# Kernel tuning notes

Hardware: AMD Instinct MI355X
Metric: run time of the kernel (lower is better)

Reference implementation:

```python
import jax, jax.numpy as jnp
import numpy as np
from jax import lax

L = 2048        # leaves per tree
VOCAB = 50000
IN_DIM = 300
MEM = 150
HID = 50
NCLS = 5


def _balanced_tree(n_leaf):
    # children-before-parent topological order; node ids: [0, n_leaf) leaves,
    # [n_leaf, 2*n_leaf-1) internal, last id is the root's single child (ROOT is passthrough).
    level = list(range(n_leaf)); nid = n_leaf; lefts = []; rights = []
    while len(level) > 1:
        nxt = []
        for j in range(0, len(level) - 1, 2):
            lefts.append(level[j]); rights.append(level[j + 1]); nxt.append(nid); nid += 1
        if len(level) % 2:
            nxt.append(level[-1])
        level = nxt
    return np.asarray(lefts, np.int32), np.asarray(rights, np.int32)


def setup_inputs() -> dict:
    key = jax.random.key(0)
    ks = jax.random.split(key, 12)
    left, right = _balanced_tree(L)
    s = 0.05
    return {
        "l_tokens": jax.random.randint(ks[0], (L,), 0, VOCAB, dtype=jnp.int32),
        "r_tokens": jax.random.randint(ks[1], (L,), 0, VOCAB, dtype=jnp.int32),
        "left_idx": jnp.asarray(left),
        "right_idx": jnp.asarray(right),
        "emb": jax.random.normal(ks[2], (VOCAB, IN_DIM), jnp.float32) * s,
        "W_ioux": jax.random.normal(ks[3], (IN_DIM, 3 * MEM), jnp.float32) * s,
        "b_ioux": jnp.zeros((3 * MEM,), jnp.float32),
        "W_iouh": jax.random.normal(ks[4], (MEM, 3 * MEM), jnp.float32) * s,
        "b_iouh": jnp.zeros((3 * MEM,), jnp.float32),
        "W_fx": jax.random.normal(ks[5], (IN_DIM, MEM), jnp.float32) * s,
        "b_fx": jnp.zeros((MEM,), jnp.float32),
        "W_fh": jax.random.normal(ks[6], (MEM, MEM), jnp.float32) * s,
        "b_fh": jnp.zeros((MEM,), jnp.float32),
        "W_attn": jax.random.normal(ks[7], (2 * MEM, MEM), jnp.float32) * s,
        "b_attn": jnp.zeros((MEM,), jnp.float32),
        "W_wh": jax.random.normal(ks[8], (2 * MEM, HID), jnp.float32) * s,
        "b_wh": jnp.zeros((HID,), jnp.float32),
        "W_wp": jax.random.normal(ks[9], (HID, NCLS), jnp.float32) * s,
        "b_wp": jnp.zeros((NCLS,), jnp.float32),
    }


def _gates(iou):
    i, o, u = jnp.split(iou, 3, axis=-1)
    return jax.nn.sigmoid(i), jax.nn.sigmoid(o), jnp.tanh(u)


def _tree_lstm(tokens, left, right, emb, W_ioux, b_ioux, W_iouh, b_iouh, W_fh, b_fh):
    # Leaves (child_c = child_h = 0): iou = ioux(x) + iouh(0); fc term vanishes.
    x = emb[tokens]                                   # [L, in_dim]
    i, o, u = _gates(x @ W_ioux + b_ioux + b_iouh)
    c_leaf = i * u
    h_leaf = o * jnp.tanh(c_leaf)
    n_leaf = tokens.shape[0]
    N = 2 * n_leaf - 1
    C = jnp.zeros((N, MEM), x.dtype).at[:n_leaf].set(c_leaf)
    H = jnp.zeros((N, MEM), x.dtype).at[:n_leaf].set(h_leaf)

    # Internal nodes (inputs=None branch): iou = iouh(sum h_child); f_k = sigmoid(fh(h_k)).
    def step(carry, inp):
        C, H = carry
        k, li, ri = inp
        hl, hr = H[li], H[ri]
        i, o, u = _gates((hl + hr) @ W_iouh + b_iouh)
        fl = jax.nn.sigmoid(hl @ W_fh + b_fh)
        fr = jax.nn.sigmoid(hr @ W_fh + b_fh)
        c = i * u + fl * C[li] + fr * C[ri]
        h = o * jnp.tanh(c)
        return (C.at[k].set(c), H.at[k].set(h)), None

    ids = jnp.arange(n_leaf, N, dtype=jnp.int32)
    (C, H), _ = lax.scan(step, (C, H), (ids, left, right))
    return H  # [N, MEM]; H[-1] is the root hidden state (ROOT is passthrough)


def reference(l_tokens, r_tokens, left_idx, right_idx, emb, W_ioux, b_ioux, W_iouh, b_iouh, W_fx, b_fx, W_fh, b_fh, W_attn, b_attn, W_wh, b_wh, W_wp, b_wp):
    Hl = _tree_lstm(l_tokens, left_idx, right_idx, emb, W_ioux, b_ioux, W_iouh, b_iouh, W_fh, b_fh)
    Hr = _tree_lstm(r_tokens, left_idx, right_idx, emb, W_ioux, b_ioux, W_iouh, b_iouh, W_fh, b_fh)
    # Soft cross-attention over all node hidden states (torch code builds [Nr,Nl,m] beta;
    # here expressed as matmuls -- identical math).
    scores = Hl @ Hr.T                               # [Nl, Nr]
    beta_sum = jax.nn.softmax(scores, axis=1) @ Hr    # [Nl, MEM]
    alpha_sum = jax.nn.softmax(scores.T, axis=1) @ Hl  # [Nr, MEM]
    v_l = jnp.concatenate([Hl, beta_sum], axis=1) @ W_attn + b_attn
    v_r = jnp.concatenate([Hr, alpha_sum], axis=1) @ W_attn + b_attn
    lh = v_l[-1:]  # root hidden (root_idx is the root's matched row)
    rh = v_r[-1:]
    feats = jnp.concatenate([lh * rh, jnp.abs(lh - rh)], axis=1)
    hid = jax.nn.sigmoid(feats @ W_wh + b_wh)
    return jax.nn.log_softmax(hid @ W_wp + b_wp, axis=-1)  # [1, NCLS]
```

## Files before the change

kernel.cpp:

```cpp
#include <hip/hip_runtime.h>
#include <math.h>

#define LEAVES 2048
#define NN     4095
#define MEMD   150
#define IOUD   450
#define IND    300
#define STR    152
#define CT     4096
#define NT     29
#define KT     10
#define KT5    5
#define NTW    39
#define LTILES 49
#define OUTSTR 788

__device__ __forceinline__ float sigf(float x) { return 1.f / (1.f + expf(-x)); }

__device__ __forceinline__ unsigned short f2bf(float v) {
    union { float f; unsigned u; } x; x.f = v;
    unsigned r = x.u + 0x7fffu + ((x.u >> 16) & 1u);
    return (unsigned short)(r >> 16);
}

typedef short bf16x8 __attribute__((ext_vector_type(8)));
typedef float f32x4  __attribute__((ext_vector_type(4)));

#define J_PW  22500
#define J_PB  (NT * KT * 64)
#define J_PBW (NTW * KT5 * 64)
#define J_XB  (4096 * 80)
__global__ __launch_bounds__(256) void k_prep(
    const float* __restrict__ Wh, const float* __restrict__ Wf,
    const float* __restrict__ Wx,
    const int* __restrict__ ltok, const int* __restrict__ rtok,
    const float* __restrict__ emb,
    float4* __restrict__ PWhf, unsigned short* __restrict__ PB,
    unsigned short* __restrict__ PBW, unsigned short* __restrict__ Xb)
{
    int i = blockIdx.x * 256 + threadIdx.x;
    if (i < J_PW) {
        int k = i / 150, d = i - k * 150;
        float4 v;
        v.x = Wh[k * IOUD + d];
        v.y = Wh[k * IOUD + 150 + d];
        v.z = Wh[k * IOUD + 300 + d];
        v.w = Wf[k * MEMD + d];
        PWhf[i] = v;
    } else if (i < J_PW + J_PB) {
        int j2 = i - J_PW;
        int nt = j2 / (KT * 64);
        int rem = j2 - nt * (KT * 64);
        int kt = rem >> 6, l = rem & 63;
        int jc = nt * 16 + (l & 15);
        int kb = kt * 32 + ((l >> 4) << 3);
        unsigned short o[8];
        #pragma unroll
        for (int e = 0; e < 8; ++e) {
            int k = kb + e;
            float v = (k < IND && jc < IOUD) ? Wx[k * IOUD + jc] : 0.f;
            o[e] = f2bf(v);
        }
        *(ushort4*)(PB + (size_t)j2 * 8)     = make_ushort4(o[0], o[1], o[2], o[3]);
        *(ushort4*)(PB + (size_t)j2 * 8 + 4) = make_ushort4(o[4], o[5], o[6], o[7]);
    } else if (i < J_PW + J_PB + J_PBW) {
        int j3 = i - J_PW - J_PB;
        int bt = j3 / (KT5 * 64);
        int rem = j3 - bt * (KT5 * 64);
        int kt = rem >> 6, l = rem & 63;
        int jc = bt * 16 + (l & 15);
        int kb = kt * 32 + ((l >> 4) << 3);
        unsigned short o[8];
        #pragma unroll
        for (int e = 0; e < 8; ++e) {
            int k = kb + e;
            float v = 0.f;
            if (k < MEMD) {
                if (jc < IOUD)                  v = Wh[k * IOUD + jc];
                else if (jc >= 464 && jc < 614) v = Wf[k * MEMD + (jc - 464)];
            }
            o[e] = f2bf(v);
        }
        *(ushort4*)(PBW + (size_t)j3 * 8)     = make_ushort4(o[0], o[1], o[2], o[3]);
        *(ushort4*)(PBW + (size_t)j3 * 8 + 4) = make_ushort4(o[4], o[5], o[6], o[7]);
    } else if (i < J_PW + J_PB + J_PBW + J_XB) {
        int idx = i - J_PW - J_PB - J_PBW;
        int row = idx / 80, q = idx - row * 80;
        int kb = q * 4;
        int leaf = row & 2047, tree = row >> 11;
        int tk = (tree ? rtok : ltok)[leaf];
        unsigned short o[4];
        #pragma unroll
        for (int e = 0; e < 4; ++e) {
            int k = kb + e;
            float v = (k < IND) ? emb[(size_t)tk * IND + k] : 0.f;
            o[e] = f2bf(v);
        }
        *(ushort4*)(Xb + (size_t)row * 320 + kb) = make_ushort4(o[0], o[1], o[2], o[3]);
    }
}

__global__ __launch_bounds__(512) void k_leafg(
    const unsigned short* __restrict__ Xb, const unsigned short* __restrict__ PB,
    const float* __restrict__ bx, const float* __restrict__ bh,
    float* __restrict__ C, float* __restrict__ H)
{
    __shared__ float ioub[16][464];
    const int t = threadIdx.x, w = t >> 6, l = t & 63;
    const int mt = blockIdx.x;

    const short* Ap = (const short*)Xb + (size_t)(mt * 16 + (l & 15)) * 320 + ((l >> 4) << 3);
    for (int nt = w; nt < NT; nt += 8) {
        const short* Bp = (const short*)PB + (size_t)nt * (KT * 512) + l * 8;
        f32x4 acc = {0.f, 0.f, 0.f, 0.f};
        #pragma unroll
        for (int kt = 0; kt < KT; ++kt) {
            bf16x8 a = *(const bf16x8*)(Ap + kt * 32);
            bf16x8 b = *(const bf16x8*)(Bp + kt * 512);
            acc = __builtin_amdgcn_mfma_f32_16x16x32_bf16(a, b, acc, 0, 0, 0);
        }
        const int col = nt * 16 + (l & 15);
        const int rb  = (l >> 4) << 2;
        #pragma unroll
        for (int r = 0; r < 4; ++r) ioub[rb + r][col] = acc[r];
    }
    __syncthreads();

    for (int idx = t; idx < 16 * MEMD; idx += 512) {
        int m = idx / MEMD, d = idx - m * MEMD;
        int gm = mt * 16 + m;
        int tree = gm >> 11, leaf = gm & 2047;
        float iv = ioub[m][d]       + bx[d]       + bh[d];
        float ov = ioub[m][d + 150] + bx[d + 150] + bh[d + 150];
        float uv = ioub[m][d + 300] + bx[d + 300] + bh[d + 300];
        float c = sigf(iv) * tanhf(uv);
        float h = sigf(ov) * tanhf(c);
        C[((size_t)tree * CT + leaf) * STR + d] = c;
        H[((size_t)tree * CT + leaf) * STR + d] = h;
    }
}

__global__ __launch_bounds__(256) void k_lvlgF(
    const unsigned short* __restrict__ PBW,
    const float* __restrict__ bh, const float* __restrict__ bf,
    float* __restrict__ C, float* __restrict__ H,
    int n, int PB_, int CB)
{
    __shared__ unsigned short AS[KT5 * 64 * 8];
    __shared__ unsigned short AL[KT5 * 64 * 8];
    __shared__ float outb[16][OUTSTR];
    const int t = threadIdx.x;
    const int m0 = blockIdx.x * 16;

    for (int s = t; s < KT5 * 64; s += 256) {
        int kt = s >> 6, l = s & 63;
        int m = m0 + (l & 15);
        int tree = (m >= n) ? 1 : 0;
        int p = m - tree * n;
        const float* rL = H + ((size_t)tree * CT + (CB + 2 * p)) * STR;
        const float* rR = rL + STR;
        int kb = kt * 32 + ((l >> 4) << 3);
        unsigned short hs8[8], hl8[8];
        if (kb + 8 <= MEMD) {
            float4 a0 = *(const float4*)(rL + kb);
            float4 a1 = *(const float4*)(rL + kb + 4);
            float4 b0 = *(const float4*)(rR + kb);
            float4 b1 = *(const float4*)(rR + kb + 4);
            float av[8] = {a0.x,a0.y,a0.z,a0.w,a1.x,a1.y,a1.z,a1.w};
            float bv[8] = {b0.x,b0.y,b0.z,b0.w,b1.x,b1.y,b1.z,b1.w};
            #pragma unroll
            for (int e = 0; e < 8; ++e) {
                hs8[e] = f2bf(av[e] + bv[e]);
                hl8[e] = f2bf(av[e]);
            }
        } else {
            #pragma unroll
            for (int e = 0; e < 8; ++e) {
                int k = kb + e;
                float a = (k < MEMD) ? rL[k] : 0.f;
                float b = (k < MEMD) ? rR[k] : 0.f;
                hs8[e] = f2bf(a + b);
                hl8[e] = f2bf(a);
            }
        }
        *(ushort4*)(AS + (size_t)s * 8)     = make_ushort4(hs8[0], hs8[1], hs8[2], hs8[3]);
        *(ushort4*)(AS + (size_t)s * 8 + 4) = make_ushort4(hs8[4], hs8[5], hs8[6], hs8[7]);
        *(ushort4*)(AL + (size_t)s * 8)     = make_ushort4(hl8[0], hl8[1], hl8[2], hl8[3]);
        *(ushort4*)(AL + (size_t)s * 8 + 4) = make_ushort4(hl8[4], hl8[5], hl8[6], hl8[7]);
    }
    __syncthreads();

    {
        const int w = t >> 6, l = t & 63;
        for (int T = w; T < LTILES; T += 4) {
            const int isHL = (T >= NTW) ? 1 : 0;
            const int bT = isHL ? (T - NTW + 29) : T;
            const unsigned short* As = isHL ? AL : AS;
            const short* Bp = (const short*)PBW + (size_t)bT * (KT5 * 512) + l * 8;
            f32x4 acc = {0.f, 0.f, 0.f, 0.f};
            #pragma unroll
            for (int kt = 0; kt < KT5; ++kt) {
                bf16x8 a = *(const bf16x8*)((const short*)As + (kt * 64 + l) * 8);
                bf16x8 b = *(const bf16x8*)(Bp + kt * 512);
                acc = __builtin_amdgcn_mfma_f32_16x16x32_bf16(a, b, acc, 0, 0, 0);
            }
            const int col = bT * 16 + (l & 15) + (isHL ? 160 : 0);
            const int rb  = (l >> 4) << 2;
            #pragma unroll
            for (int r = 0; r < 4; ++r) outb[rb + r][col] = acc[r];
        }
    }
    __syncthreads();

    for (int idx = t; idx < 16 * MEMD; idx += 256) {
        int m = idx / MEMD, d = idx - m * MEMD;
        int gm = m0 + m;
        int tree = (gm >= n) ? 1 : 0, p = gm - tree * n;
        float* Ct = C + (size_t)tree * CT * STR;
        float* Ht = H + (size_t)tree * CT * STR;
        int c0 = CB + 2 * p;
        float cl = Ct[(size_t)c0 * STR + d];
        float cr = Ct[(size_t)(c0 + 1) * STR + d];
        float iv = outb[m][d]       + bh[d];
        float ov = outb[m][d + 150] + bh[d + 150];
        float uv = outb[m][d + 300] + bh[d + 300];
        float fs = outb[m][464 + d] + 2.f * bf[d];
        float fl = outb[m][624 + d] + bf[d];
        float fr = fs - fl;
        float c = sigf(iv) * tanhf(uv) + sigf(fl) * cl + sigf(fr) * cr;
        float h = sigf(ov) * tanhf(c);
        size_t rw = (size_t)(PB_ + p) * STR + d;
        Ct[rw] = c;
        Ht[rw] = h;
    }
}

__global__ __launch_bounds__(640) void k_node(
    const float4* __restrict__ PWhf, const float* __restrict__ bh,
    const float* __restrict__ bf,
    float* __restrict__ C, float* __restrict__ H, int PB_, int CB)
{
    __shared__ float hsv[MEMD], hlv[MEMD];
    __shared__ float part[4][5][152];
    const int tree = blockIdx.y, node = blockIdx.x, t = threadIdx.x;
    float* Ct = C + (size_t)tree * CT * STR;
    float* Ht = H + (size_t)tree * CT * STR;
    const int c0 = CB + 2 * node;

    if (t < MEMD) {
        float a = Ht[(size_t)c0 * STR + t];
        float b = Ht[(size_t)(c0 + 1) * STR + t];
        hsv[t] = a + b;
        hlv[t] = a;
    }
    __syncthreads();

    const int grp = t / 160, d = t - grp * 160;
    if (d < MEMD) {
        const int k0 = (grp * MEMD) >> 2;
        const int k1 = ((grp + 1) * MEMD) >> 2;
        float ai = 0.f, ao = 0.f, au = 0.f, afs = 0.f, afl = 0.f;
        const float4* wp = PWhf + d;
        #pragma unroll 4
        for (int k = k0; k < k1; ++k) {
            float4 w = wp[(size_t)k * 150];
            float hs = hsv[k], hl = hlv[k];
            ai  = fmaf(hs, w.x, ai);
            ao  = fmaf(hs, w.y, ao);
            au  = fmaf(hs, w.z, au);
            afs = fmaf(hs, w.w, afs);
            afl = fmaf(hl, w.w, afl);
        }
        part[grp][0][d] = ai;  part[grp][1][d] = ao;  part[grp][2][d] = au;
        part[grp][3][d] = afs; part[grp][4][d] = afl;
    }
    __syncthreads();

    if (t < MEMD) {
        const int d2 = t;
        float ai = bh[d2], ao = bh[d2 + 150], au = bh[d2 + 300];
        float bfv = bf[d2];
        float afs = 2.f * bfv, afl = bfv;
        #pragma unroll
        for (int g = 0; g < 4; ++g) {
            ai  += part[g][0][d2]; ao  += part[g][1][d2]; au += part[g][2][d2];
            afs += part[g][3][d2]; afl += part[g][4][d2];
        }
        float cl = Ct[(size_t)c0 * STR + d2];
        float cr = Ct[(size_t)(c0 + 1) * STR + d2];
        float frv = afs - afl;
        float c = sigf(ai) * tanhf(au) + sigf(afl) * cl + sigf(frv) * cr;
        float h = sigf(ao) * tanhf(c);
        size_t rw = (size_t)(PB_ + node) * STR + d2;
        Ct[rw] = c;
        Ht[rw] = h;
    }
}

__global__ __launch_bounds__(256) void k_attn(
    const float* __restrict__ H, float* __restrict__ cstat, float* __restrict__ part)
{
    __shared__ float lv[MEMD];
    __shared__ float sc[64];
    __shared__ float pv[64];
    const int bid = blockIdx.x, t = threadIdx.x;
    const int side = bid >> 6, chunk = bid & 63;
    const int j0 = chunk << 6;
    const int jn = min(64, NN - j0);
    const float* lastrow = H + ((size_t)side * CT + (NN - 1)) * STR;
    if (t < MEMD) lv[t] = lastrow[t];
    __syncthreads();

    const float* src = H + (size_t)(side ^ 1) * CT * STR + (size_t)j0 * STR;
    const int wave = t >> 6, lane = t & 63;
    for (int r = wave; r < jn; r += 4) {
        const float* row = src + (size_t)r * STR;
        float a = lv[lane] * row[lane] + lv[lane + 64] * row[lane + 64];
        if (lane < 22) a += lv[lane + 128] * row[lane + 128];
        #pragma unroll
        for (int off = 32; off; off >>= 1) a += __shfl_xor(a, off);
        if (lane == 0) sc[r] = a;
    }
    __syncthreads();
    if (wave == 0) {
        float v = (lane < jn) ? sc[lane] : -3.4e38f;
        float m = v;
        #pragma unroll
        for (int off = 32; off; off >>= 1) m = fmaxf(m, __shfl_xor(m, off));
        float e = (lane < jn) ? expf(v - m) : 0.f;
        pv[lane] = e;
        float s = e;
        #pragma unroll
        for (int off = 32; off; off >>= 1) s += __shfl_xor(s, off);
        if (lane == 0) {
            cstat[(side * 64 + chunk) * 2 + 0] = m;
            cstat[(side * 64 + chunk) * 2 + 1] = s;
        }
    }
    __syncthreads();
    if (t < MEMD) {
        float a = 0.f;
        for (int j = 0; j < jn; ++j) a += pv[j] * src[(size_t)j * STR + t];
        part[(size_t)(side * 64 + chunk) * STR + t] = a;
    }
}

__global__ __launch_bounds__(512) void k_final(
    const float* __restrict__ H, const float* __restrict__ cstat,
    const float* __restrict__ part,
    const float* __restrict__ Wattn, const float* __restrict__ battn,
    const float* __restrict__ Wwh, const float* __restrict__ bwh,
    const float* __restrict__ Wwp, const float* __restrict__ bwp,
    float* __restrict__ outp)
{
    __shared__ float scl[2][64];
    __shared__ float gseS[2];
    __shared__ float ba[300], catl[300], catr[300], vl[150], vr[150];
    __shared__ float feats[300], hid[50], logits[5];
    const int t = threadIdx.x, wave = t >> 6, lane = t & 63;

    if (wave < 2) {
        float lm = cstat[(wave * 64 + lane) * 2 + 0];
        float ls = cstat[(wave * 64 + lane) * 2 + 1];
        float m = lm;
        #pragma unroll
        for (int off = 32; off; off >>= 1) m = fmaxf(m, __shfl_xor(m, off));
        float s = expf(lm - m);
        scl[wave][lane] = s;
        float se = ls * s;
        #pragma unroll
        for (int off = 32; off; off >>= 1) se += __shfl_xor(se, off);
        if (lane == 0) gseS[wave] = se;
    }
    __syncthreads();
    if (t < 300) {
        int side = t / MEMD, d = t - side * MEMD;
        float a = 0.f;
        for (int c = 0; c < 64; ++c)
            a += part[(size_t)(side * 64 + c) * STR + d] * scl[side][c];
        ba[t] = a / gseS[side];
    }
    __syncthreads();
    const float* Hl_last = H + (size_t)(0 * CT + NN - 1) * STR;
    const float* Hr_last = H + (size_t)(1 * CT + NN - 1) * STR;
    if (t < MEMD) {
        catl[t] = Hl_last[t]; catl[150 + t] = ba[t];
        catr[t] = Hr_last[t]; catr[150 + t] = ba[150 + t];
    }
    __syncthreads();
    if (t < 300) {
        int d = (t < 150) ? t : t - 150;
        const float* cat = (t < 150) ? catl : catr;
        float a = battn[d];
        for (int k = 0; k < 300; ++k) a = fmaf(cat[k], Wattn[k * 150 + d], a);
        if (t < 150) vl[d] = a; else vr[d] = a;
    }
    __syncthreads();
    if (t < MEMD) {
        feats[t] = vl[t] * vr[t];
        feats[150 + t] = fabsf(vl[t] - vr[t]);
    }
    __syncthreads();
    if (t < 50) {
        float a = bwh[t];
        for (int k = 0; k < 300; ++k) a = fmaf(feats[k], Wwh[k * 50 + t], a);
        hid[t] = sigf(a);
    }
    __syncthreads();
    if (t < 5) {
        float a = bwp[t];
        for (int g = 0; g < 50; ++g) a = fmaf(hid[g], Wwp[g * 5 + t], a);
        logits[t] = a;
    }
    __syncthreads();
    if (t == 0) {
        float m = logits[0];
        for (int c = 1; c < 5; ++c) m = fmaxf(m, logits[c]);
        float s = 0.f;
        for (int c = 0; c < 5; ++c) s += expf(logits[c] - m);
        float lse = m + logf(s);
        for (int c = 0; c < 5; ++c) outp[c] = logits[c] - lse;
    }
}

extern "C" void kernel_launch(void* const* d_in, const int* in_sizes, int n_in,
                              void* d_out, int out_size, void* d_ws, size_t ws_size,
                              hipStream_t stream)
{
    const int*   ltok  = (const int*)d_in[0];
    const int*   rtok  = (const int*)d_in[1];
    const float* emb   = (const float*)d_in[4];
    const float* Wx    = (const float*)d_in[5];
    const float* bx    = (const float*)d_in[6];
    const float* Wh    = (const float*)d_in[7];
    const float* bh    = (const float*)d_in[8];
    const float* Wf    = (const float*)d_in[11];
    const float* bf    = (const float*)d_in[12];
    const float* Wattn = (const float*)d_in[13];
    const float* battn = (const float*)d_in[14];
    const float* Wwh   = (const float*)d_in[15];
    const float* bwh   = (const float*)d_in[16];
    const float* Wwp   = (const float*)d_in[17];
    const float* bwp   = (const float*)d_in[18];
    float* out = (float*)d_out;

    float* ws    = (float*)d_ws;
    float*  C    = ws;
    float*  H    = C + (size_t)2 * CT * STR;
    float*  cs   = H + (size_t)2 * CT * STR;
    float*  part = cs + 256;
    float4* PWhf = (float4*)(part + (size_t)128 * STR);
    unsigned short* Xb  = (unsigned short*)(PWhf + 22500);
    unsigned short* PBb = Xb + (size_t)4096 * 320;
    unsigned short* PBW = PBb + (size_t)NT * KT * 512;

    const int prep_items = J_PW + J_PB + J_PBW + J_XB;
    k_prep<<<dim3((prep_items + 255) / 256), dim3(256), 0, stream>>>(
        Wh, Wf, Wx, ltok, rtok, emb, PWhf, PBb, PBW, Xb);

    k_leafg<<<dim3(256), dim3(512), 0, stream>>>(Xb, PBb, bx, bh, C, H);

    k_lvlgF<<<dim3(128), dim3(256), 0, stream>>>(PBW, bh, bf, C, H, 1024, 2048, 0);
    k_lvlgF<<<dim3(64),  dim3(256), 0, stream>>>(PBW, bh, bf, C, H, 512, 3072, 2048);
    k_lvlgF<<<dim3(32),  dim3(256), 0, stream>>>(PBW, bh, bf, C, H, 256, 3584, 3072);

    k_node<<<dim3(128, 2), dim3(640), 0, stream>>>(PWhf, bh, bf, C, H, 3840, 3584);
    k_node<<<dim3(64,  2), dim3(640), 0, stream>>>(PWhf, bh, bf, C, H, 3968, 3840);
    k_node<<<dim3(32,  2), dim3(640), 0, stream>>>(PWhf, bh, bf, C, H, 4032, 3968);
    k_node<<<dim3(16,  2), dim3(640), 0, stream>>>(PWhf, bh, bf, C, H, 4064, 4032);
    k_node<<<dim3(8,   2), dim3(640), 0, stream>>>(PWhf, bh, bf, C, H, 4080, 4064);
    k_node<<<dim3(4,   2), dim3(640), 0, stream>>>(PWhf, bh, bf, C, H, 4088, 4080);
    k_node<<<dim3(2,   2), dim3(640), 0, stream>>>(PWhf, bh, bf, C, H, 4092, 4088);
    k_node<<<dim3(1,   2), dim3(640), 0, stream>>>(PWhf, bh, bf, C, H, 4094, 4092);

    k_attn<<<dim3(128), dim3(256), 0, stream>>>(H, cs, part);
    k_final<<<dim3(1), dim3(512), 0, stream>>>(H, cs, part, Wattn, battn,
                                               Wwh, bwh, Wwp, bwp, out);
}
```

Measured before the change: 142.4 us.

## Fuse last five tree levels into one persistent block per tree

Replaces five small per-level k_node launches for the top of the tree with a single kernel launch in which one 1024-thread block per tree walks the five levels, using __syncthreads between levels. The aim is to remove the launch and inter-kernel gap overhead of tiny kernels. In exchange, each level runs on only one CU per tree, with one thread per (node, dim) doing a full 150-long dot product. That reduces parallelism compared with the split-K k_node design.

```diff
diff --git a/kernel.cpp b/kernel.cpp
--- a/kernel.cpp
+++ b/kernel.cpp
@@ -297,6 +297,62 @@
     }
 }
 
+__global__ __launch_bounds__(1024) void k_tail5(
+    const float4* __restrict__ PWhf, const float* __restrict__ bh,
+    const float* __restrict__ bf,
+    float* __restrict__ C, float* __restrict__ H)
+{
+    __shared__ float hsv[16][152], hlv[16][152];
+    const int tree = blockIdx.x, t = threadIdx.x;
+    float* Ct = C + (size_t)tree * CT * STR;
+    float* Ht = H + (size_t)tree * CT * STR;
+
+    const int ns[5]  = {16, 8, 4, 2, 1};
+    const int cbs[5] = {4032, 4064, 4080, 4088, 4092};
+    const int pbs[5] = {4064, 4080, 4088, 4092, 4094};
+
+    #pragma unroll 1
+    for (int lv = 0; lv < 5; ++lv) {
+        const int n = ns[lv], CB = cbs[lv], PB_ = pbs[lv];
+        for (int idx = t; idx < n * MEMD; idx += 1024) {
+            int p = idx / MEMD, d = idx - p * MEMD;
+            float a = Ht[(size_t)(CB + 2 * p) * STR + d];
+            float b = Ht[(size_t)(CB + 2 * p + 1) * STR + d];
+            hsv[p][d] = a + b;
+            hlv[p][d] = a;
+        }
+        __syncthreads();
+        for (int idx = t; idx < n * MEMD; idx += 1024) {
+            int p = idx / MEMD, d = idx - p * MEMD;
+            float ai = bh[d], ao = bh[d + 150], au = bh[d + 300];
+            float bfv = bf[d];
+            float afs = 2.f * bfv, afl = bfv;
+            const float4* wp = PWhf + d;
+            const float* hsp = hsv[p];
+            const float* hlp = hlv[p];
+            #pragma unroll 5
+            for (int k = 0; k < MEMD; ++k) {
+                float4 w = wp[(size_t)k * 150];
+                float hs = hsp[k], hl = hlp[k];
+                ai  = fmaf(hs, w.x, ai);
+                ao  = fmaf(hs, w.y, ao);
+                au  = fmaf(hs, w.z, au);
+                afs = fmaf(hs, w.w, afs);
+                afl = fmaf(hl, w.w, afl);
+            }
+            float cl = Ct[(size_t)(CB + 2 * p) * STR + d];
+            float cr = Ct[(size_t)(CB + 2 * p + 1) * STR + d];
+            float frv = afs - afl;
+            float c = sigf(ai) * tanhf(au) + sigf(afl) * cl + sigf(frv) * cr;
+            float h = sigf(ao) * tanhf(c);
+            size_t rw = (size_t)(PB_ + p) * STR + d;
+            Ct[rw] = c;
+            Ht[rw] = h;
+        }
+        __syncthreads();
+    }
+}
+
 __global__ __launch_bounds__(256) void k_attn(
     const float* __restrict__ H, float* __restrict__ cstat, float* __restrict__ part)
 {
@@ -467,11 +523,8 @@
     k_node<<<dim3(128, 2), dim3(640), 0, stream>>>(PWhf, bh, bf, C, H, 3840, 3584);
     k_node<<<dim3(64,  2), dim3(640), 0, stream>>>(PWhf, bh, bf, C, H, 3968, 3840);
     k_node<<<dim3(32,  2), dim3(640), 0, stream>>>(PWhf, bh, bf, C, H, 4032, 3968);
-    k_node<<<dim3(16,  2), dim3(640), 0, stream>>>(PWhf, bh, bf, C, H, 4064, 4032);
-    k_node<<<dim3(8,   2), dim3(640), 0, stream>>>(PWhf, bh, bf, C, H, 4080, 4064);
-    k_node<<<dim3(4,   2), dim3(640), 0, stream>>>(PWhf, bh, bf, C, H, 4088, 4080);
-    k_node<<<dim3(2,   2), dim3(640), 0, stream>>>(PWhf, bh, bf, C, H, 4092, 4088);
-    k_node<<<dim3(1,   2), dim3(640), 0, stream>>>(PWhf, bh, bf, C, H, 4094, 4092);
+
+    k_tail5<<<dim3(2), dim3(1024), 0, stream>>>(PWhf, bh, bf, C, H);
 
     k_attn<<<dim3(128), dim3(256), 0, stream>>>(H, cs, part);
     k_final<<<dim3(1), dim3(512), 0, stream>>>(H, cs, part, Wattn, battn,
```

Result: slower. 206.6 us (+45.1%).
